# Kernel optimization log

Measured on AMD Instinct MI355X. Metric: run time of the kernel, lower is better.

## Reference

```python
import jax, jax.numpy as jnp
import numpy as np

NPOINT, RADIUS, NSAMPLE = 1024, 0.2, 32
ALPHA, EPS = 0.2, 1e-5  # leaky-relu slope, BN eps


def index_points(points, idx):
    # points [B,N,C], idx [B,...] int -> [B,...,C]
    return jax.vmap(lambda p, i: p[i])(points, idx)


def farthest_point_sample(xyz, npoint):
    # xyz [B,N,3] -> idx [B,npoint]; deterministic start at index 0
    B, N, _ = xyz.shape

    def step(carry, _):
        dist, far = carry
        centroid = jnp.take_along_axis(xyz, far[:, None, None], axis=1)  # [B,1,3]
        d = jnp.sum((xyz - centroid) ** 2, -1)                           # [B,N]
        dist = jnp.minimum(dist, d)
        return (dist, jnp.argmax(dist, -1).astype(jnp.int32)), far

    init = (jnp.full((B, N), 1e10, xyz.dtype), jnp.zeros((B,), jnp.int32))
    _, idxs = jax.lax.scan(step, init, None, length=npoint)
    return idxs.T  # [B, npoint]


def square_distance(src, dst):
    d = -2.0 * jnp.einsum('bnc,bmc->bnm', src, dst)
    d = d + jnp.sum(src ** 2, -1)[:, :, None]
    d = d + jnp.sum(dst ** 2, -1)[:, None, :]
    return d


def query_ball_point(radius, nsample, xyz, new_xyz):
    B, N, _ = xyz.shape
    sqr = square_distance(new_xyz, xyz)  # [B,S,N]
    gi = jnp.where(sqr > radius ** 2, N, jnp.arange(N, dtype=jnp.int32)[None, None, :])
    gi = jnp.sort(gi, axis=-1)[:, :, :nsample]  # [B,S,K]
    first = gi[:, :, :1]
    return jnp.where(gi == N, first, gi)


def mlp_bn_relu(x, W, b, g, be, m, v):
    # 1x1 conv + eval-mode BatchNorm + ReLU; x [..., Cin]
    y = jnp.einsum('...i,oi->...o', x, W) + b
    y = (y - m) * (g / jnp.sqrt(v + EPS)) + be
    return jax.nn.relu(y)


def _forward(xyz, points, W0, b0, g0, be0, m0, v0, W1, b1, g1, be1, m1, v1,
             W2, b2, g2, be2, m2, v2, a):
    xyz_t = jnp.transpose(xyz, (0, 2, 1))     # [B,N,3]
    pts = jnp.transpose(points, (0, 2, 1))    # [B,N,D]

    fps_idx = farthest_point_sample(xyz_t, NPOINT)          # [B,S]
    new_xyz = index_points(xyz_t, fps_idx)                  # [B,S,3]
    idx = query_ball_point(RADIUS, NSAMPLE, xyz_t, new_xyz)  # [B,S,K]
    grouped_xyz = index_points(xyz_t, idx)                  # [B,S,K,3]
    grouped_norm = grouped_xyz - new_xyz[:, :, None, :]
    grouped_pts = index_points(pts, idx)                    # [B,S,K,D]
    fps_points = jnp.concatenate([new_xyz, index_points(pts, fps_idx)], -1)  # [B,S,3+D]
    new_points = jnp.concatenate([grouped_norm, grouped_pts], -1)            # [B,S,K,3+D]

    layers = [(W0, b0, g0, be0, m0, v0), (W1, b1, g1, be1, m1, v1),
              (W2, b2, g2, be2, m2, v2)]
    for (W, b, g, be, m, v) in layers:
        fps_points = mlp_bn_relu(fps_points, W, b, g, be, m, v)
        new_points = mlp_bn_relu(new_points, W, b, g, be, m, v)

    # graph attention pooling over neighbors (dim K)
    delta_p = new_xyz[:, :, None, :] - grouped_xyz                      # [B,S,K,3]
    delta_h = fps_points[:, :, None, :] - new_points                    # [B,S,K,F]
    e = jax.nn.leaky_relu(
        jnp.einsum('bskc,cf->bskf', jnp.concatenate([delta_p, delta_h], -1), a),
        ALPHA)
    att = jax.nn.softmax(e, axis=2)                                     # softmax over K
    pooled = jnp.sum(att * new_points, axis=2)                          # [B,S,F]
    return jnp.transpose(new_xyz, (0, 2, 1)), jnp.transpose(pooled, (0, 2, 1))


def setup_inputs() -> dict:
    key = jax.random.key(0)
    ks = jax.random.split(key, 32)
    d = {}
    d['xyz'] = jax.random.uniform(ks[0], (16, 3, 4096), jnp.float32)
    d['points'] = jax.random.normal(ks[1], (16, 6, 4096), jnp.float32)
    dims = [(9, 64), (64, 64), (64, 128)]
    for li, (ci, co) in enumerate(dims):
        d[f'W{li}'] = jax.random.normal(ks[2 + 6 * li], (co, ci), jnp.float32) * (1.0 / np.sqrt(ci))
        d[f'b{li}'] = jax.random.normal(ks[3 + 6 * li], (co,), jnp.float32) * 0.05
        d[f'g{li}'] = jax.random.uniform(ks[4 + 6 * li], (co,), jnp.float32, 0.5, 1.5)
        d[f'be{li}'] = jax.random.normal(ks[5 + 6 * li], (co,), jnp.float32) * 0.05
        d[f'm{li}'] = jax.random.normal(ks[6 + 6 * li], (co,), jnp.float32) * 0.05
        d[f'v{li}'] = jax.random.uniform(ks[7 + 6 * li], (co,), jnp.float32, 0.5, 1.5)
    d['a'] = jax.random.normal(ks[20], (131, 128), jnp.float32) * 0.1
    return d


def reference(xyz, points, W0, b0, g0, be0, m0, v0, W1, b1, g1, be1, m1, v1,
              W2, b2, g2, be2, m2, v2, a):
    return _forward(xyz, points, W0, b0, g0, be0, m0, v0, W1, b1, g1, be1,
                    m1, v1, W2, b2, g2, be2, m2, v2, a)
```

## Files before the change

### kernel.cpp

```cpp
#include <hip/hip_runtime.h>

#define BB 16
#define NN 4096
#define SS 1024
#define KNB 32

#define FPSIDX_OFF 0
#define GIDX_OFF   (BB*SS)
#define NORM_OFF   (GIDX_OFF + BB*SS*KNB)
#define FPIN_OFF   (NORM_OFF + BB*NN)
#define WF_OFF     (FPIN_OFF + BB*SS*9)

#define W0T 0
#define B0F 576
#define W1T 640
#define B1F 4736
#define W2T 4800
#define B2F 12992

__global__ __launch_bounds__(128) void k_fold(
    const float* W0,const float* b0,const float* g0,const float* be0,const float* m0,const float* v0,
    const float* W1,const float* b1,const float* g1,const float* be1,const float* m1,const float* v1,
    const float* W2,const float* b2,const float* g2,const float* be2,const float* m2,const float* v2,
    float* wf){
  int t = threadIdx.x;
  if (t < 64){
    float s = g0[t]/sqrtf(v0[t]+1e-5f);
    wf[B0F+t] = (b0[t]-m0[t])*s + be0[t];
    for (int c=0;c<9;c++) wf[W0T + c*64 + t] = W0[t*9+c]*s;
    float s1 = g1[t]/sqrtf(v1[t]+1e-5f);
    wf[B1F+t] = (b1[t]-m1[t])*s1 + be1[t];
    for (int c=0;c<64;c++) wf[W1T + c*64 + t] = W1[t*64+c]*s1;
  }
  if (t < 128){
    float s2 = g2[t]/sqrtf(v2[t]+1e-5f);
    wf[B2F+t] = (b2[t]-m2[t])*s2 + be2[t];
    for (int c=0;c<64;c++) wf[W2T + c*128 + t] = W2[t*64+c]*s2;
  }
}

__global__ __launch_bounds__(256) void k_norm(const float* xyz, float* nrm){
  int i = blockIdx.x*256 + threadIdx.x;
  int b = i >> 12, n = i & (NN-1);
  const float* X = xyz + (size_t)b*3*NN;
  float x=X[n], y=X[NN+n], z=X[2*NN+n];
  nrm[i] = __fadd_rn(__fadd_rn(__fmul_rn(x,x),__fmul_rn(y,y)),__fmul_rn(z,z));
}

template<int CTRL, int RMASK>
__device__ __forceinline__ void dpp_max_step(unsigned &lo, unsigned &hi){
  unsigned nlo = (unsigned)__builtin_amdgcn_update_dpp(0, (int)lo, CTRL, RMASK, 0xF, false);
  unsigned nhi = (unsigned)__builtin_amdgcn_update_dpp(0, (int)hi, CTRL, RMASK, 0xF, false);
  unsigned long long cand = ((unsigned long long)nhi<<32) | nlo;
  unsigned long long curk = ((unsigned long long)hi<<32)  | lo;
  if (cand > curk){ lo = nlo; hi = nhi; }
}

__global__ __launch_bounds__(256) void k_fps(const float* xyz, int* fpsidx){
  __shared__ float px[NN], py[NN], pz[NN];
  __shared__ unsigned long long red[2][4];
  int b = blockIdx.x, tid = threadIdx.x;
  int w = tid >> 6, lane = tid & 63;
  const float* X = xyz + (size_t)b*3*NN;
  float lx[16], ly[16], lz[16], dist[16];
  #pragma unroll
  for (int j=0;j<16;j++){
    int p = tid + j*256;
    float x = X[p], y = X[NN+p], z = X[2*NN+p];
    px[p]=x; py[p]=y; pz[p]=z;
    lx[j]=x; ly[j]=y; lz[j]=z; dist[j]=1e10f;
  }
  if (tid==0) fpsidx[b*SS] = 0;
  __syncthreads();
  int cur = 0;
  for (int t=1;t<SS;t++){
    float cx=px[cur], cy=py[cur], cz=pz[cur];
    float bv = -1.0f; int bj = 0;
    #pragma unroll
    for (int j=0;j<16;j++){
      float dx=__fsub_rn(lx[j],cx), dy=__fsub_rn(ly[j],cy), dz=__fsub_rn(lz[j],cz);
      float d = __fadd_rn(__fadd_rn(__fmul_rn(dx,dx),__fmul_rn(dy,dy)),__fmul_rn(dz,dz));
      float nd = fminf(dist[j], d);
      dist[j] = nd;
      bool c = nd > bv;
      bv = c ? nd : bv;
      bj = c ? j  : bj;
    }
    int bi = tid + (bj << 8);
    unsigned lo = 0xFFFFFFFFu - (unsigned)bi;
    unsigned hi = __float_as_uint(bv);
    dpp_max_step<0x111,0xF>(lo,hi);
    dpp_max_step<0x112,0xF>(lo,hi);
    dpp_max_step<0x114,0xF>(lo,hi);
    dpp_max_step<0x118,0xF>(lo,hi);
    dpp_max_step<0x142,0xA>(lo,hi);
    dpp_max_step<0x143,0xC>(lo,hi);
    unsigned glo = (unsigned)__builtin_amdgcn_readlane((int)lo, 63);
    unsigned ghi = (unsigned)__builtin_amdgcn_readlane((int)hi, 63);
    if (lane==0) red[t&1][w] = ((unsigned long long)ghi<<32) | glo;
    __syncthreads();
    unsigned long long k0 = red[t&1][0], k1 = red[t&1][1];
    unsigned long long k2 = red[t&1][2], k3 = red[t&1][3];
    unsigned long long bk = k0;
    if (k1 > bk) bk = k1;
    if (k2 > bk) bk = k2;
    if (k3 > bk) bk = k3;
    cur = (int)(0xFFFFFFFFu - (unsigned)(bk & 0xFFFFFFFFull));
    if (tid==0) fpsidx[b*SS+t] = cur;
  }
}

__global__ __launch_bounds__(256) void k_ball(const float* xyz, const float* points, const float* nrm,
                                              const int* fpsidx, int* gidx, float* fpin, float* out0){
  int wid = threadIdx.x >> 6, lane = threadIdx.x & 63;
  int s = blockIdx.x*4 + wid;
  int b = s >> 10, si = s & (SS-1);
  const float* X = xyz + (size_t)b*3*NN;
  int cidx = fpsidx[s];
  float sx = X[cidx], sy = X[NN+cidx], sz = X[2*NN+cidx];
  float sn = nrm[b*NN + cidx];
  if (lane < 3){
    float v = lane==0?sx:(lane==1?sy:sz);
    fpin[s*9+lane] = v;
    out0[b*3*SS + lane*SS + si] = v;
  } else if (lane < 9){
    fpin[s*9+lane] = points[(size_t)b*6*NN + (size_t)(lane-3)*NN + cidx];
  }
  const float R2 = (float)(0.2*0.2);
  int total = 0; int first = 0;
  for (int ch=0; ch<NN/64; ch++){
    int n = ch*64 + lane;
    float pxv=X[n], pyv=X[NN+n], pzv=X[2*NN+n];
    float dot = __fmaf_rn(sz,pzv, __fmaf_rn(sy,pyv, __fmul_rn(sx,pxv)));
    float sqr = __fadd_rn(__fadd_rn(__fmul_rn(-2.0f,dot), sn), nrm[b*NN+n]);
    bool inc = (sqr <= R2);
    unsigned long long mask = __ballot(inc);
    if (total == 0 && mask != 0ull) first = ch*64 + (__ffsll((long long)mask) - 1);
    if (inc){
      int pos = total + __popcll(mask & ((1ull<<lane)-1ull));
      if (pos < KNB) gidx[s*KNB + pos] = n;
    }
    total += (int)__popcll(mask);
    if (total >= KNB) break;
  }
  if (total < KNB && lane >= total && lane < KNB) gidx[s*KNB + lane] = first;
}

__global__ __launch_bounds__(256) void k_fused(const float* __restrict__ xyz,
                                               const float* __restrict__ points,
                                               const float* __restrict__ am,
                                               const float* __restrict__ wf,
                                               const int* __restrict__ gidx,
                                               const float* __restrict__ fpin,
                                               float* __restrict__ out1){
  __shared__ float smem[64*68*2];
  __shared__ float Hf1[2][64], Hf2[2][64], F3l[2][128];
  float* H1  = smem;
  float* H2  = smem + 64*68;
  float* DNP = smem;

  int tid  = threadIdx.x;
  int lane = tid & 63;
  int k    = lane & 31;
  int ctr  = lane >> 5;
  int wv   = __builtin_amdgcn_readfirstlane(tid >> 6);
  int s0   = blockIdx.x*2;
  int s    = s0 + ctr;
  int b    = s >> 10;
  int si   = s & (SS-1);
  int row  = lane;

  int ki = gidx[s*KNB + k];
  const float* X = xyz + (size_t)b*3*NN;
  const float* P = points + (size_t)b*6*NN;
  float fin0 = fpin[s*9+0], fin1 = fpin[s*9+1], fin2 = fpin[s*9+2];
  float gx0 = X[ki]      - fin0;
  float gx1 = X[NN+ki]   - fin1;
  float gx2 = X[2*NN+ki] - fin2;
  float g3 = P[ki], g4 = P[NN+ki], g5 = P[2*NN+ki];
  float g6 = P[3*NN+ki], g7 = P[4*NN+ki], g8 = P[5*NN+ki];

  {
    int f0 = wv*16;
    float acc[16];
    #pragma unroll
    for (int j=0;j<16;j++) acc[j] = wf[B0F + f0 + j];
    #pragma unroll
    for (int c=0;c<9;c++){
      float xv = (c==0)?gx0:(c==1)?gx1:(c==2)?gx2:(c==3)?g3:(c==4)?g4:(c==5)?g5:(c==6)?g6:(c==7)?g7:g8;
      const float* wr = wf + W0T + c*64 + f0;
      #pragma unroll
      for (int j=0;j<16;j++) acc[j] = fmaf(xv, wr[j], acc[j]);
    }
    #pragma unroll
    for (int j=0;j<16;j+=4){
      float4 o; o.x=fmaxf(acc[j],0.f); o.y=fmaxf(acc[j+1],0.f);
      o.z=fmaxf(acc[j+2],0.f); o.w=fmaxf(acc[j+3],0.f);
      *(float4*)&H1[row*68 + f0 + j] = o;
    }
  }
  if (tid < 128){
    int f = tid & 63; int cf = tid >> 6;
    int sf = s0 + cf;
    float acc = wf[B0F + f];
    #pragma unroll
    for (int c=0;c<9;c++) acc = fmaf(fpin[sf*9+c], wf[W0T + c*64 + f], acc);
    Hf1[cf][f] = fmaxf(acc, 0.0f);
  }
  __syncthreads();

  {
    int f0 = wv*16;
    float acc[16];
    #pragma unroll
    for (int j=0;j<16;j++) acc[j] = wf[B1F + f0 + j];
    #pragma unroll 8
    for (int c4=0;c4<16;c4++){
      float4 hv = *(const float4*)&H1[row*68 + c4*4];
      const float* wr = wf + W1T + c4*4*64 + f0;
      #pragma unroll
      for (int j=0;j<16;j++) acc[j] = fmaf(hv.x, wr[j],     acc[j]);
      #pragma unroll
      for (int j=0;j<16;j++) acc[j] = fmaf(hv.y, wr[64+j],  acc[j]);
      #pragma unroll
      for (int j=0;j<16;j++) acc[j] = fmaf(hv.z, wr[128+j], acc[j]);
      #pragma unroll
      for (int j=0;j<16;j++) acc[j] = fmaf(hv.w, wr[192+j], acc[j]);
    }
    #pragma unroll
    for (int j=0;j<16;j+=4){
      float4 o; o.x=fmaxf(acc[j],0.f); o.y=fmaxf(acc[j+1],0.f);
      o.z=fmaxf(acc[j+2],0.f); o.w=fmaxf(acc[j+3],0.f);
      *(float4*)&H2[row*68 + f0 + j] = o;
    }
  }
  if (tid < 128){
    int f = tid & 63; int cf = tid >> 6;
    float acc = wf[B1F + f];
    #pragma unroll 16
    for (int c=0;c<64;c++) acc = fmaf(Hf1[cf][c], wf[W1T + c*64 + f], acc);
    Hf2[cf][f] = fmaxf(acc, 0.0f);
  }
  __syncthreads();

  float np[32];
  {
    int f0 = wv*32;
    #pragma unroll
    for (int j=0;j<32;j++) np[j] = wf[B2F + f0 + j];
    #pragma unroll 4
    for (int c4=0;c4<16;c4++){
      float4 hv = *(const float4*)&H2[row*68 + c4*4];
      const float* wr = wf + W2T + c4*4*128 + f0;
      #pragma unroll
      for (int j=0;j<32;j++) np[j] = fmaf(hv.x, wr[j],     np[j]);
      #pragma unroll
      for (int j=0;j<32;j++) np[j] = fmaf(hv.y, wr[128+j], np[j]);
      #pragma unroll
      for (int j=0;j<32;j++) np[j] = fmaf(hv.z, wr[256+j], np[j]);
      #pragma unroll
      for (int j=0;j<32;j++) np[j] = fmaf(hv.w, wr[384+j], np[j]);
    }
    #pragma unroll
    for (int j=0;j<32;j++) np[j] = fmaxf(np[j], 0.0f);
  }
  {
    int f = tid & 127; int cf = tid >> 7;
    float acc = wf[B2F + f];
    #pragma unroll 16
    for (int c=0;c<64;c++) acc = fmaf(Hf2[cf][c], wf[W2T + c*128 + f], acc);
    F3l[cf][f] = fmaxf(acc, 0.0f);
  }
  __syncthreads();

  {
    int f0 = wv*32;
    #pragma unroll
    for (int j=0;j<32;j+=4){
      float4 d;
      d.x = F3l[ctr][f0+j]   - np[j];
      d.y = F3l[ctr][f0+j+1] - np[j+1];
      d.z = F3l[ctr][f0+j+2] - np[j+2];
      d.w = F3l[ctr][f0+j+3] - np[j+3];
      *(float4*)&DNP[row*132 + f0 + j] = d;
    }
  }
  __syncthreads();

  {
    float dp0 = -gx0, dp1 = -gx1, dp2 = -gx2;
    size_t ob = (size_t)b*128*SS + si;
    #pragma unroll
    for (int p=0;p<4;p++){
      int f0 = wv*32 + p*8;
      float e[8];
      const float* a0 = am + f0;
      #pragma unroll
      for (int j=0;j<8;j++)
        e[j] = fmaf(dp2, a0[256+j], fmaf(dp1, a0[128+j], dp0*a0[j]));
      #pragma unroll 4
      for (int c4=0;c4<32;c4++){
        float4 dv = *(const float4*)&DNP[row*132 + c4*4];
        const float* wr = am + (3 + c4*4)*128 + f0;
        #pragma unroll
        for (int j=0;j<8;j++) e[j] = fmaf(dv.x, wr[j],     e[j]);
        #pragma unroll
        for (int j=0;j<8;j++) e[j] = fmaf(dv.y, wr[128+j], e[j]);
        #pragma unroll
        for (int j=0;j<8;j++) e[j] = fmaf(dv.z, wr[256+j], e[j]);
        #pragma unroll
        for (int j=0;j<8;j++) e[j] = fmaf(dv.w, wr[384+j], e[j]);
      }
      #pragma unroll
      for (int j=0;j<8;j++){
        float ej = e[j]; ej = (ej >= 0.0f) ? ej : 0.2f*ej;
        float mx = ej;
        mx = fmaxf(mx, __shfl_xor(mx,1));
        mx = fmaxf(mx, __shfl_xor(mx,2));
        mx = fmaxf(mx, __shfl_xor(mx,4));
        mx = fmaxf(mx, __shfl_xor(mx,8));
        mx = fmaxf(mx, __shfl_xor(mx,16));
        float pp = __expf(ej - mx);
        float sm = pp;
        sm += __shfl_xor(sm,1); sm += __shfl_xor(sm,2); sm += __shfl_xor(sm,4);
        sm += __shfl_xor(sm,8); sm += __shfl_xor(sm,16);
        float po = (pp / sm) * np[p*8+j];
        po += __shfl_xor(po,1); po += __shfl_xor(po,2); po += __shfl_xor(po,4);
        po += __shfl_xor(po,8); po += __shfl_xor(po,16);
        if (k == 0) out1[ob + (size_t)(f0+j)*SS] = po;
      }
    }
  }
}

extern "C" void kernel_launch(void* const* d_in, const int* in_sizes, int n_in,
                              void* d_out, int out_size, void* d_ws, size_t ws_size,
                              hipStream_t stream){
  (void)in_sizes; (void)n_in; (void)out_size; (void)ws_size;
  const float* xyz    = (const float*)d_in[0];
  const float* points = (const float*)d_in[1];
  const float* am     = (const float*)d_in[20];
  float* ws  = (float*)d_ws;
  int*   fpsidx = (int*)d_ws + FPSIDX_OFF;
  int*   gidx   = (int*)d_ws + GIDX_OFF;
  float* nrm    = ws + NORM_OFF;
  float* fpin   = ws + FPIN_OFF;
  float* wf     = ws + WF_OFF;
  float* out0   = (float*)d_out;
  float* out1   = (float*)d_out + BB*3*SS;

  k_fold<<<1,128,0,stream>>>(
      (const float*)d_in[2],(const float*)d_in[3],(const float*)d_in[4],(const float*)d_in[5],(const float*)d_in[6],(const float*)d_in[7],
      (const float*)d_in[8],(const float*)d_in[9],(const float*)d_in[10],(const float*)d_in[11],(const float*)d_in[12],(const float*)d_in[13],
      (const float*)d_in[14],(const float*)d_in[15],(const float*)d_in[16],(const float*)d_in[17],(const float*)d_in[18],(const float*)d_in[19],
      wf);
  k_norm<<<BB*NN/256,256,0,stream>>>(xyz, nrm);
  k_fps<<<BB,256,0,stream>>>(xyz, fpsidx);
  k_ball<<<BB*SS/4,256,0,stream>>>(xyz, points, nrm, fpsidx, gidx, fpin, out0);
  k_fused<<<BB*SS/2,256,0,stream>>>(xyz, points, am, wf, gidx, fpin, out1);
}
```

Before: 1.108 ms.

## Widen FPS to 512 threads with packed float2 math and float4 centroid loads

The farthest-point-sampling kernel now runs 512 threads per batch instead of 256, so each thread holds 8 points instead of 16. Distances are computed with two-wide float vectors so the compiler can emit packed FP32 instructions, with contraction disabled to keep rounding exact. The centroid is read as one float4 from shared memory right after the reduction. The aim is a shorter serial per-iteration critical path in this latency-bound 1023-step loop. In exchange the cross-wave reduction is 8-way instead of 4-way, and the barrier now spans 8 waves.

```diff
diff --git a/kernel.cpp b/kernel.cpp
--- a/kernel.cpp
+++ b/kernel.cpp
@@ -17,6 +17,8 @@
 #define B1F 4736
 #define W2T 4800
 #define B2F 12992
+
+typedef float v2f __attribute__((ext_vector_type(2)));
 
 __global__ __launch_bounds__(128) void k_fold(
     const float* W0,const float* b0,const float* g0,const float* be0,const float* m0,const float* v0,
@@ -56,37 +58,46 @@
   if (cand > curk){ lo = nlo; hi = nhi; }
 }
 
-__global__ __launch_bounds__(256) void k_fps(const float* xyz, int* fpsidx){
-  __shared__ float px[NN], py[NN], pz[NN];
-  __shared__ unsigned long long red[2][4];
+__global__ __launch_bounds__(512) void k_fps(const float* xyz, int* fpsidx){
+  #pragma clang fp contract(off)
+  __shared__ float4 pxyz4[NN];
+  __shared__ unsigned long long red[2][8];
   int b = blockIdx.x, tid = threadIdx.x;
   int w = tid >> 6, lane = tid & 63;
   const float* X = xyz + (size_t)b*3*NN;
-  float lx[16], ly[16], lz[16], dist[16];
+  v2f lx[4], ly[4], lz[4], dist[4];
   #pragma unroll
-  for (int j=0;j<16;j++){
-    int p = tid + j*256;
-    float x = X[p], y = X[NN+p], z = X[2*NN+p];
-    px[p]=x; py[p]=y; pz[p]=z;
-    lx[j]=x; ly[j]=y; lz[j]=z; dist[j]=1e10f;
+  for (int m=0;m<4;m++){
+    int p0 = tid + (2*m)*512, p1 = tid + (2*m+1)*512;
+    float x0=X[p0], y0=X[NN+p0], z0=X[2*NN+p0];
+    float x1=X[p1], y1=X[NN+p1], z1=X[2*NN+p1];
+    float4 q0; q0.x=x0; q0.y=y0; q0.z=z0; q0.w=0.f;
+    float4 q1; q1.x=x1; q1.y=y1; q1.z=z1; q1.w=0.f;
+    pxyz4[p0] = q0; pxyz4[p1] = q1;
+    lx[m].x=x0; lx[m].y=x1; ly[m].x=y0; ly[m].y=y1; lz[m].x=z0; lz[m].y=z1;
+    dist[m].x=1e10f; dist[m].y=1e10f;
   }
   if (tid==0) fpsidx[b*SS] = 0;
-  __syncthreads();
-  int cur = 0;
+  float cx = X[0], cy = X[NN], cz = X[2*NN];
+  __syncthreads();
   for (int t=1;t<SS;t++){
-    float cx=px[cur], cy=py[cur], cz=pz[cur];
+    v2f cxx, cyy, czz;
+    cxx.x=cx; cxx.y=cx; cyy.x=cy; cyy.y=cy; czz.x=cz; czz.y=cz;
     float bv = -1.0f; int bj = 0;
     #pragma unroll
-    for (int j=0;j<16;j++){
-      float dx=__fsub_rn(lx[j],cx), dy=__fsub_rn(ly[j],cy), dz=__fsub_rn(lz[j],cz);
-      float d = __fadd_rn(__fadd_rn(__fmul_rn(dx,dx),__fmul_rn(dy,dy)),__fmul_rn(dz,dz));
-      float nd = fminf(dist[j], d);
-      dist[j] = nd;
-      bool c = nd > bv;
-      bv = c ? nd : bv;
-      bj = c ? j  : bj;
-    }
-    int bi = tid + (bj << 8);
+    for (int m=0;m<4;m++){
+      v2f dx = lx[m]-cxx, dy = ly[m]-cyy, dz = lz[m]-czz;
+      v2f dd = (dx*dx + dy*dy) + dz*dz;
+      v2f nd; nd.x = fminf(dist[m].x, dd.x); nd.y = fminf(dist[m].y, dd.y);
+      dist[m] = nd;
+      bool pc = nd.y > nd.x;
+      float vm = pc ? nd.y : nd.x;
+      int   jm = pc ? (2*m+1) : (2*m);
+      bool c = vm > bv;
+      bv = c ? vm : bv;
+      bj = c ? jm : bj;
+    }
+    int bi = tid + (bj << 9);
     unsigned lo = 0xFFFFFFFFu - (unsigned)bi;
     unsigned hi = __float_as_uint(bv);
     dpp_max_step<0x111,0xF>(lo,hi);
@@ -101,11 +112,18 @@
     __syncthreads();
     unsigned long long k0 = red[t&1][0], k1 = red[t&1][1];
     unsigned long long k2 = red[t&1][2], k3 = red[t&1][3];
-    unsigned long long bk = k0;
-    if (k1 > bk) bk = k1;
-    if (k2 > bk) bk = k2;
-    if (k3 > bk) bk = k3;
-    cur = (int)(0xFFFFFFFFu - (unsigned)(bk & 0xFFFFFFFFull));
+    unsigned long long k4 = red[t&1][4], k5 = red[t&1][5];
+    unsigned long long k6 = red[t&1][6], k7 = red[t&1][7];
+    unsigned long long a0 = (k1>k0)?k1:k0;
+    unsigned long long a1 = (k3>k2)?k3:k2;
+    unsigned long long a2 = (k5>k4)?k5:k4;
+    unsigned long long a3 = (k7>k6)?k7:k6;
+    unsigned long long b0 = (a1>a0)?a1:a0;
+    unsigned long long b1 = (a3>a2)?a3:a2;
+    unsigned long long bk = (b1>b0)?b1:b0;
+    int cur = (int)(0xFFFFFFFFu - (unsigned)(bk & 0xFFFFFFFFull));
+    float4 cc = pxyz4[cur];
+    cx = cc.x; cy = cc.y; cz = cc.z;
     if (tid==0) fpsidx[b*SS+t] = cur;
   }
 }
@@ -355,7 +373,7 @@
       (const float*)d_in[14],(const float*)d_in[15],(const float*)d_in[16],(const float*)d_in[17],(const float*)d_in[18],(const float*)d_in[19],
       wf);
   k_norm<<<BB*NN/256,256,0,stream>>>(xyz, nrm);
-  k_fps<<<BB,256,0,stream>>>(xyz, fpsidx);
+  k_fps<<<BB,512,0,stream>>>(xyz, fpsidx);
   k_ball<<<BB*SS/4,256,0,stream>>>(xyz, points, nrm, fpsidx, gidx, fpin, out0);
   k_fused<<<BB*SS/2,256,0,stream>>>(xyz, points, am, wf, gidx, fpin, out1);
 }
```

Measured after the change: 1.200 ms. 8.3% more time.

## Fuse FPS, ball query and MLP into persistent producer-consumer megakernel

Applied to the files above, without the earlier changes.

Merges the FPS, ball-query and fused MLP/attention kernels into a single persistent kernel. Sixteen blocks run FPS and publish each centroid index with atomic stores, while the other 944 blocks spin-wait on those indices so ball query and MLP overlap the serial FPS. The FPS loop now carries the winning point's coordinates through the DPP reduction, which drops the shared-memory coordinate lookup each step. Group indices and centroid features stay in LDS instead of going through global memory. The risks are deadlock if the FPS blocks are not all resident alongside the spinning consumers, and ordering that depends on relaxed atomics.

```diff
diff --git a/kernel.cpp b/kernel.cpp
--- a/kernel.cpp
+++ b/kernel.cpp
@@ -5,11 +5,12 @@
 #define SS 1024
 #define KNB 32
 
+#define NCONS 944
+#define NBLK (NCONS + 16)
+
 #define FPSIDX_OFF 0
-#define GIDX_OFF   (BB*SS)
-#define NORM_OFF   (GIDX_OFF + BB*SS*KNB)
-#define FPIN_OFF   (NORM_OFF + BB*NN)
-#define WF_OFF     (FPIN_OFF + BB*SS*9)
+#define NORM_OFF   (BB*SS)
+#define WF_OFF     (NORM_OFF + BB*NN)
 
 #define W0T 0
 #define B0F 576
@@ -48,288 +49,316 @@
 }
 
 template<int CTRL, int RMASK>
-__device__ __forceinline__ void dpp_max_step(unsigned &lo, unsigned &hi){
-  unsigned nlo = (unsigned)__builtin_amdgcn_update_dpp(0, (int)lo, CTRL, RMASK, 0xF, false);
-  unsigned nhi = (unsigned)__builtin_amdgcn_update_dpp(0, (int)hi, CTRL, RMASK, 0xF, false);
+__device__ __forceinline__ void dpp5(unsigned &klo, unsigned &khi, float &x, float &y, float &z){
+  unsigned nlo = (unsigned)__builtin_amdgcn_update_dpp(0, (int)klo, CTRL, RMASK, 0xF, false);
+  unsigned nhi = (unsigned)__builtin_amdgcn_update_dpp(0, (int)khi, CTRL, RMASK, 0xF, false);
+  int nx = __builtin_amdgcn_update_dpp(0, __float_as_int(x), CTRL, RMASK, 0xF, false);
+  int ny = __builtin_amdgcn_update_dpp(0, __float_as_int(y), CTRL, RMASK, 0xF, false);
+  int nz = __builtin_amdgcn_update_dpp(0, __float_as_int(z), CTRL, RMASK, 0xF, false);
   unsigned long long cand = ((unsigned long long)nhi<<32) | nlo;
-  unsigned long long curk = ((unsigned long long)hi<<32)  | lo;
-  if (cand > curk){ lo = nlo; hi = nhi; }
-}
-
-__global__ __launch_bounds__(256) void k_fps(const float* xyz, int* fpsidx){
-  __shared__ float px[NN], py[NN], pz[NN];
-  __shared__ unsigned long long red[2][4];
-  int b = blockIdx.x, tid = threadIdx.x;
-  int w = tid >> 6, lane = tid & 63;
-  const float* X = xyz + (size_t)b*3*NN;
-  float lx[16], ly[16], lz[16], dist[16];
-  #pragma unroll
-  for (int j=0;j<16;j++){
-    int p = tid + j*256;
-    float x = X[p], y = X[NN+p], z = X[2*NN+p];
-    px[p]=x; py[p]=y; pz[p]=z;
-    lx[j]=x; ly[j]=y; lz[j]=z; dist[j]=1e10f;
-  }
-  if (tid==0) fpsidx[b*SS] = 0;
-  __syncthreads();
-  int cur = 0;
-  for (int t=1;t<SS;t++){
-    float cx=px[cur], cy=py[cur], cz=pz[cur];
-    float bv = -1.0f; int bj = 0;
+  unsigned long long curk = ((unsigned long long)khi<<32) | klo;
+  if (cand > curk){
+    klo=nlo; khi=nhi;
+    x=__int_as_float(nx); y=__int_as_float(ny); z=__int_as_float(nz);
+  }
+}
+
+__global__ __launch_bounds__(256, 4) void k_mega(const float* __restrict__ xyz,
+                                                 const float* __restrict__ points,
+                                                 const float* __restrict__ am,
+                                                 const float* __restrict__ wf,
+                                                 const float* __restrict__ nrm,
+                                                 int* fpsidx,
+                                                 float* __restrict__ out0,
+                                                 float* __restrict__ out1){
+  __shared__ float smem[64*68*2];
+  __shared__ float Hf1[2][64], Hf2[2][64], F3l[2][128];
+  __shared__ int   gidx_l[2][KNB];
+  __shared__ float fpin_l[2][12];
+  __shared__ unsigned long long rkey[2][4];
+  __shared__ float4 rxyz[2][4];
+
+  int tid  = threadIdx.x;
+  int lane = tid & 63;
+  int w    = tid >> 6;
+
+  if (blockIdx.x < 16){
+    int b = blockIdx.x;
+    const float* X = xyz + (size_t)b*3*NN;
+    float lx[16], ly[16], lz[16], dist[16];
     #pragma unroll
     for (int j=0;j<16;j++){
-      float dx=__fsub_rn(lx[j],cx), dy=__fsub_rn(ly[j],cy), dz=__fsub_rn(lz[j],cz);
-      float d = __fadd_rn(__fadd_rn(__fmul_rn(dx,dx),__fmul_rn(dy,dy)),__fmul_rn(dz,dz));
-      float nd = fminf(dist[j], d);
-      dist[j] = nd;
-      bool c = nd > bv;
-      bv = c ? nd : bv;
-      bj = c ? j  : bj;
-    }
-    int bi = tid + (bj << 8);
-    unsigned lo = 0xFFFFFFFFu - (unsigned)bi;
-    unsigned hi = __float_as_uint(bv);
-    dpp_max_step<0x111,0xF>(lo,hi);
-    dpp_max_step<0x112,0xF>(lo,hi);
-    dpp_max_step<0x114,0xF>(lo,hi);
-    dpp_max_step<0x118,0xF>(lo,hi);
-    dpp_max_step<0x142,0xA>(lo,hi);
-    dpp_max_step<0x143,0xC>(lo,hi);
-    unsigned glo = (unsigned)__builtin_amdgcn_readlane((int)lo, 63);
-    unsigned ghi = (unsigned)__builtin_amdgcn_readlane((int)hi, 63);
-    if (lane==0) red[t&1][w] = ((unsigned long long)ghi<<32) | glo;
-    __syncthreads();
-    unsigned long long k0 = red[t&1][0], k1 = red[t&1][1];
-    unsigned long long k2 = red[t&1][2], k3 = red[t&1][3];
-    unsigned long long bk = k0;
-    if (k1 > bk) bk = k1;
-    if (k2 > bk) bk = k2;
-    if (k3 > bk) bk = k3;
-    cur = (int)(0xFFFFFFFFu - (unsigned)(bk & 0xFFFFFFFFull));
-    if (tid==0) fpsidx[b*SS+t] = cur;
-  }
-}
-
-__global__ __launch_bounds__(256) void k_ball(const float* xyz, const float* points, const float* nrm,
-                                              const int* fpsidx, int* gidx, float* fpin, float* out0){
-  int wid = threadIdx.x >> 6, lane = threadIdx.x & 63;
-  int s = blockIdx.x*4 + wid;
-  int b = s >> 10, si = s & (SS-1);
-  const float* X = xyz + (size_t)b*3*NN;
-  int cidx = fpsidx[s];
-  float sx = X[cidx], sy = X[NN+cidx], sz = X[2*NN+cidx];
-  float sn = nrm[b*NN + cidx];
-  if (lane < 3){
-    float v = lane==0?sx:(lane==1?sy:sz);
-    fpin[s*9+lane] = v;
-    out0[b*3*SS + lane*SS + si] = v;
-  } else if (lane < 9){
-    fpin[s*9+lane] = points[(size_t)b*6*NN + (size_t)(lane-3)*NN + cidx];
-  }
-  const float R2 = (float)(0.2*0.2);
-  int total = 0; int first = 0;
-  for (int ch=0; ch<NN/64; ch++){
-    int n = ch*64 + lane;
-    float pxv=X[n], pyv=X[NN+n], pzv=X[2*NN+n];
-    float dot = __fmaf_rn(sz,pzv, __fmaf_rn(sy,pyv, __fmul_rn(sx,pxv)));
-    float sqr = __fadd_rn(__fadd_rn(__fmul_rn(-2.0f,dot), sn), nrm[b*NN+n]);
-    bool inc = (sqr <= R2);
-    unsigned long long mask = __ballot(inc);
-    if (total == 0 && mask != 0ull) first = ch*64 + (__ffsll((long long)mask) - 1);
-    if (inc){
-      int pos = total + __popcll(mask & ((1ull<<lane)-1ull));
-      if (pos < KNB) gidx[s*KNB + pos] = n;
-    }
-    total += (int)__popcll(mask);
-    if (total >= KNB) break;
-  }
-  if (total < KNB && lane >= total && lane < KNB) gidx[s*KNB + lane] = first;
-}
-
-__global__ __launch_bounds__(256) void k_fused(const float* __restrict__ xyz,
-                                               const float* __restrict__ points,
-                                               const float* __restrict__ am,
-                                               const float* __restrict__ wf,
-                                               const int* __restrict__ gidx,
-                                               const float* __restrict__ fpin,
-                                               float* __restrict__ out1){
-  __shared__ float smem[64*68*2];
-  __shared__ float Hf1[2][64], Hf2[2][64], F3l[2][128];
+      int p = tid + j*256;
+      lx[j]=X[p]; ly[j]=X[NN+p]; lz[j]=X[2*NN+p]; dist[j]=1e10f;
+    }
+    if (tid==0)
+      __hip_atomic_store((unsigned*)&fpsidx[b*SS], 0u, __ATOMIC_RELAXED, __HIP_MEMORY_SCOPE_AGENT);
+    float cx = X[0], cy = X[NN], cz = X[2*NN];
+    __syncthreads();
+    for (int t=1;t<SS;t++){
+      float bv = -1.0f, bx = 0.f, by = 0.f, bz = 0.f; int bj = 0;
+      #pragma unroll
+      for (int j=0;j<16;j++){
+        float dx=__fsub_rn(lx[j],cx), dy=__fsub_rn(ly[j],cy), dz=__fsub_rn(lz[j],cz);
+        float d = __fadd_rn(__fadd_rn(__fmul_rn(dx,dx),__fmul_rn(dy,dy)),__fmul_rn(dz,dz));
+        float nd = fminf(dist[j], d);
+        dist[j] = nd;
+        bool c = nd > bv;
+        bv = c ? nd : bv;
+        bj = c ? j  : bj;
+        bx = c ? lx[j] : bx; by = c ? ly[j] : by; bz = c ? lz[j] : bz;
+      }
+      int bi = tid + (bj << 8);
+      unsigned klo = 0xFFFFFFFFu - (unsigned)bi;
+      unsigned khi = __float_as_uint(bv);
+      dpp5<0x111,0xF>(klo,khi,bx,by,bz);
+      dpp5<0x112,0xF>(klo,khi,bx,by,bz);
+      dpp5<0x114,0xF>(klo,khi,bx,by,bz);
+      dpp5<0x118,0xF>(klo,khi,bx,by,bz);
+      dpp5<0x142,0xA>(klo,khi,bx,by,bz);
+      dpp5<0x143,0xC>(klo,khi,bx,by,bz);
+      unsigned glo = (unsigned)__builtin_amdgcn_readlane((int)klo, 63);
+      unsigned ghi = (unsigned)__builtin_amdgcn_readlane((int)khi, 63);
+      float wx = __int_as_float(__builtin_amdgcn_readlane(__float_as_int(bx), 63));
+      float wy = __int_as_float(__builtin_amdgcn_readlane(__float_as_int(by), 63));
+      float wz = __int_as_float(__builtin_amdgcn_readlane(__float_as_int(bz), 63));
+      int par = t & 1;
+      if (lane==0){
+        rkey[par][w] = ((unsigned long long)ghi<<32) | glo;
+        float4 q; q.x=wx; q.y=wy; q.z=wz; q.w=0.f;
+        rxyz[par][w] = q;
+      }
+      __syncthreads();
+      unsigned long long k0 = rkey[par][0], k1 = rkey[par][1];
+      unsigned long long k2 = rkey[par][2], k3 = rkey[par][3];
+      float4 c0 = rxyz[par][0], c1 = rxyz[par][1], c2 = rxyz[par][2], c3 = rxyz[par][3];
+      bool s01 = k1 > k0; unsigned long long a0 = s01?k1:k0;
+      float ax = s01?c1.x:c0.x, ay = s01?c1.y:c0.y, az = s01?c1.z:c0.z;
+      bool s23 = k3 > k2; unsigned long long a1 = s23?k3:k2;
+      float ex = s23?c3.x:c2.x, ey = s23?c3.y:c2.y, ez = s23?c3.z:c2.z;
+      bool sf = a1 > a0; unsigned long long bk = sf?a1:a0;
+      cx = sf?ex:ax; cy = sf?ey:ay; cz = sf?ez:az;
+      int cur = (int)(0xFFFFFFFFu - (unsigned)(bk & 0xFFFFFFFFull));
+      if (tid==0)
+        __hip_atomic_store((unsigned*)&fpsidx[b*SS+t], (unsigned)cur, __ATOMIC_RELAXED, __HIP_MEMORY_SCOPE_AGENT);
+    }
+    return;
+  }
+
+  int j    = blockIdx.x - 16;
+  int k    = lane & 31;
+  int ctr  = lane >> 5;
+  int wv   = __builtin_amdgcn_readfirstlane(tid >> 6);
   float* H1  = smem;
   float* H2  = smem + 64*68;
   float* DNP = smem;
-
-  int tid  = threadIdx.x;
-  int lane = tid & 63;
-  int k    = lane & 31;
-  int ctr  = lane >> 5;
-  int wv   = __builtin_amdgcn_readfirstlane(tid >> 6);
-  int s0   = blockIdx.x*2;
-  int s    = s0 + ctr;
-  int b    = s >> 10;
-  int si   = s & (SS-1);
-  int row  = lane;
-
-  int ki = gidx[s*KNB + k];
-  const float* X = xyz + (size_t)b*3*NN;
-  const float* P = points + (size_t)b*6*NN;
-  float fin0 = fpin[s*9+0], fin1 = fpin[s*9+1], fin2 = fpin[s*9+2];
-  float gx0 = X[ki]      - fin0;
-  float gx1 = X[NN+ki]   - fin1;
-  float gx2 = X[2*NN+ki] - fin2;
-  float g3 = P[ki], g4 = P[NN+ki], g5 = P[2*NN+ki];
-  float g6 = P[3*NN+ki], g7 = P[4*NN+ki], g8 = P[5*NN+ki];
-
-  {
-    int f0 = wv*16;
-    float acc[16];
-    #pragma unroll
-    for (int j=0;j<16;j++) acc[j] = wf[B0F + f0 + j];
-    #pragma unroll
-    for (int c=0;c<9;c++){
-      float xv = (c==0)?gx0:(c==1)?gx1:(c==2)?gx2:(c==3)?g3:(c==4)?g4:(c==5)?g5:(c==6)?g6:(c==7)?g7:g8;
-      const float* wr = wf + W0T + c*64 + f0;
-      #pragma unroll
-      for (int j=0;j<16;j++) acc[j] = fmaf(xv, wr[j], acc[j]);
-    }
-    #pragma unroll
-    for (int j=0;j<16;j+=4){
-      float4 o; o.x=fmaxf(acc[j],0.f); o.y=fmaxf(acc[j+1],0.f);
-      o.z=fmaxf(acc[j+2],0.f); o.w=fmaxf(acc[j+3],0.f);
-      *(float4*)&H1[row*68 + f0 + j] = o;
-    }
-  }
-  if (tid < 128){
-    int f = tid & 63; int cf = tid >> 6;
-    int sf = s0 + cf;
-    float acc = wf[B0F + f];
-    #pragma unroll
-    for (int c=0;c<9;c++) acc = fmaf(fpin[sf*9+c], wf[W0T + c*64 + f], acc);
-    Hf1[cf][f] = fmaxf(acc, 0.0f);
-  }
-  __syncthreads();
-
-  {
-    int f0 = wv*16;
-    float acc[16];
-    #pragma unroll
-    for (int j=0;j<16;j++) acc[j] = wf[B1F + f0 + j];
-    #pragma unroll 8
-    for (int c4=0;c4<16;c4++){
-      float4 hv = *(const float4*)&H1[row*68 + c4*4];
-      const float* wr = wf + W1T + c4*4*64 + f0;
-      #pragma unroll
-      for (int j=0;j<16;j++) acc[j] = fmaf(hv.x, wr[j],     acc[j]);
-      #pragma unroll
-      for (int j=0;j<16;j++) acc[j] = fmaf(hv.y, wr[64+j],  acc[j]);
-      #pragma unroll
-      for (int j=0;j<16;j++) acc[j] = fmaf(hv.z, wr[128+j], acc[j]);
-      #pragma unroll
-      for (int j=0;j<16;j++) acc[j] = fmaf(hv.w, wr[192+j], acc[j]);
-    }
-    #pragma unroll
-    for (int j=0;j<16;j+=4){
-      float4 o; o.x=fmaxf(acc[j],0.f); o.y=fmaxf(acc[j+1],0.f);
-      o.z=fmaxf(acc[j+2],0.f); o.w=fmaxf(acc[j+3],0.f);
-      *(float4*)&H2[row*68 + f0 + j] = o;
-    }
-  }
-  if (tid < 128){
-    int f = tid & 63; int cf = tid >> 6;
-    float acc = wf[B1F + f];
-    #pragma unroll 16
-    for (int c=0;c<64;c++) acc = fmaf(Hf1[cf][c], wf[W1T + c*64 + f], acc);
-    Hf2[cf][f] = fmaxf(acc, 0.0f);
-  }
-  __syncthreads();
-
-  float np[32];
-  {
-    int f0 = wv*32;
-    #pragma unroll
-    for (int j=0;j<32;j++) np[j] = wf[B2F + f0 + j];
-    #pragma unroll 4
-    for (int c4=0;c4<16;c4++){
-      float4 hv = *(const float4*)&H2[row*68 + c4*4];
-      const float* wr = wf + W2T + c4*4*128 + f0;
-      #pragma unroll
-      for (int j=0;j<32;j++) np[j] = fmaf(hv.x, wr[j],     np[j]);
-      #pragma unroll
-      for (int j=0;j<32;j++) np[j] = fmaf(hv.y, wr[128+j], np[j]);
-      #pragma unroll
-      for (int j=0;j<32;j++) np[j] = fmaf(hv.z, wr[256+j], np[j]);
-      #pragma unroll
-      for (int j=0;j<32;j++) np[j] = fmaf(hv.w, wr[384+j], np[j]);
-    }
-    #pragma unroll
-    for (int j=0;j<32;j++) np[j] = fmaxf(np[j], 0.0f);
-  }
-  {
-    int f = tid & 127; int cf = tid >> 7;
-    float acc = wf[B2F + f];
-    #pragma unroll 16
-    for (int c=0;c<64;c++) acc = fmaf(Hf2[cf][c], wf[W2T + c*128 + f], acc);
-    F3l[cf][f] = fmaxf(acc, 0.0f);
-  }
-  __syncthreads();
-
-  {
-    int f0 = wv*32;
-    #pragma unroll
-    for (int j=0;j<32;j+=4){
-      float4 d;
-      d.x = F3l[ctr][f0+j]   - np[j];
-      d.y = F3l[ctr][f0+j+1] - np[j+1];
-      d.z = F3l[ctr][f0+j+2] - np[j+2];
-      d.w = F3l[ctr][f0+j+3] - np[j+3];
-      *(float4*)&DNP[row*132 + f0 + j] = d;
-    }
-  }
-  __syncthreads();
-
-  {
-    float dp0 = -gx0, dp1 = -gx1, dp2 = -gx2;
-    size_t ob = (size_t)b*128*SS + si;
-    #pragma unroll
-    for (int p=0;p<4;p++){
-      int f0 = wv*32 + p*8;
-      float e[8];
-      const float* a0 = am + f0;
-      #pragma unroll
-      for (int j=0;j<8;j++)
-        e[j] = fmaf(dp2, a0[256+j], fmaf(dp1, a0[128+j], dp0*a0[j]));
+  int row = lane;
+
+  for (int u = j; u < BB*SS/2; u += NCONS){
+    int bb = u & 15;
+    int pp = u >> 4;
+    const float* X = xyz + (size_t)bb*3*NN;
+    const float* P = points + (size_t)bb*6*NN;
+
+    if (w < 2){
+      int si = 2*pp + w;
+      int sg = bb*SS + si;
+      int cidx;
+      for(;;){
+        unsigned v = __hip_atomic_load((const unsigned*)&fpsidx[sg], __ATOMIC_RELAXED, __HIP_MEMORY_SCOPE_AGENT);
+        if (v != 0xFFFFFFFFu){ cidx = (int)v; break; }
+        __builtin_amdgcn_s_sleep(4);
+      }
+      float sx = X[cidx], sy = X[NN+cidx], sz = X[2*NN+cidx];
+      float sn = nrm[bb*NN + cidx];
+      if (lane < 3){
+        float v = lane==0?sx:(lane==1?sy:sz);
+        fpin_l[w][lane] = v;
+        out0[bb*3*SS + lane*SS + si] = v;
+      } else if (lane < 9){
+        fpin_l[w][lane] = points[(size_t)bb*6*NN + (size_t)(lane-3)*NN + cidx];
+      }
+      const float R2 = (float)(0.2*0.2);
+      int total = 0; int first = 0;
+      for (int ch=0; ch<NN/64; ch++){
+        int n = ch*64 + lane;
+        float pxv=X[n], pyv=X[NN+n], pzv=X[2*NN+n];
+        float dot = __fmaf_rn(sz,pzv, __fmaf_rn(sy,pyv, __fmul_rn(sx,pxv)));
+        float sqr = __fadd_rn(__fadd_rn(__fmul_rn(-2.0f,dot), sn), nrm[bb*NN+n]);
+        bool inc = (sqr <= R2);
+        unsigned long long mask = __ballot(inc);
+        if (total == 0 && mask != 0ull) first = ch*64 + (__ffsll((long long)mask) - 1);
+        if (inc){
+          int pos = total + __popcll(mask & ((1ull<<lane)-1ull));
+          if (pos < KNB) gidx_l[w][pos] = n;
+        }
+        total += (int)__popcll(mask);
+        if (total >= KNB) break;
+      }
+      if (total < KNB && lane >= total && lane < KNB) gidx_l[w][lane] = first;
+    }
+    __syncthreads();
+
+    int sil = 2*pp + ctr;
+    int ki = gidx_l[ctr][k];
+    float fin0 = fpin_l[ctr][0], fin1 = fpin_l[ctr][1], fin2 = fpin_l[ctr][2];
+    float gx0 = X[ki]      - fin0;
+    float gx1 = X[NN+ki]   - fin1;
+    float gx2 = X[2*NN+ki] - fin2;
+    float g3 = P[ki], g4 = P[NN+ki], g5 = P[2*NN+ki];
+    float g6 = P[3*NN+ki], g7 = P[4*NN+ki], g8 = P[5*NN+ki];
+
+    {
+      int f0 = wv*16;
+      float acc[16];
+      #pragma unroll
+      for (int q=0;q<16;q++) acc[q] = wf[B0F + f0 + q];
+      #pragma unroll
+      for (int c=0;c<9;c++){
+        float xv = (c==0)?gx0:(c==1)?gx1:(c==2)?gx2:(c==3)?g3:(c==4)?g4:(c==5)?g5:(c==6)?g6:(c==7)?g7:g8;
+        const float* wr = wf + W0T + c*64 + f0;
+        #pragma unroll
+        for (int q=0;q<16;q++) acc[q] = fmaf(xv, wr[q], acc[q]);
+      }
+      #pragma unroll
+      for (int q=0;q<16;q+=4){
+        float4 o; o.x=fmaxf(acc[q],0.f); o.y=fmaxf(acc[q+1],0.f);
+        o.z=fmaxf(acc[q+2],0.f); o.w=fmaxf(acc[q+3],0.f);
+        *(float4*)&H1[row*68 + f0 + q] = o;
+      }
+    }
+    if (tid < 128){
+      int f = tid & 63; int cf = tid >> 6;
+      float acc = wf[B0F + f];
+      #pragma unroll
+      for (int c=0;c<9;c++) acc = fmaf(fpin_l[cf][c], wf[W0T + c*64 + f], acc);
+      Hf1[cf][f] = fmaxf(acc, 0.0f);
+    }
+    __syncthreads();
+
+    {
+      int f0 = wv*16;
+      float acc[16];
+      #pragma unroll
+      for (int q=0;q<16;q++) acc[q] = wf[B1F + f0 + q];
+      #pragma unroll 8
+      for (int c4=0;c4<16;c4++){
+        float4 hv = *(const float4*)&H1[row*68 + c4*4];
+        const float* wr = wf + W1T + c4*4*64 + f0;
+        #pragma unroll
+        for (int q=0;q<16;q++) acc[q] = fmaf(hv.x, wr[q],     acc[q]);
+        #pragma unroll
+        for (int q=0;q<16;q++) acc[q] = fmaf(hv.y, wr[64+q],  acc[q]);
+        #pragma unroll
+        for (int q=0;q<16;q++) acc[q] = fmaf(hv.z, wr[128+q], acc[q]);
+        #pragma unroll
+        for (int q=0;q<16;q++) acc[q] = fmaf(hv.w, wr[192+q], acc[q]);
+      }
+      #pragma unroll
+      for (int q=0;q<16;q+=4){
+        float4 o; o.x=fmaxf(acc[q],0.f); o.y=fmaxf(acc[q+1],0.f);
+        o.z=fmaxf(acc[q+2],0.f); o.w=fmaxf(acc[q+3],0.f);
+        *(float4*)&H2[row*68 + f0 + q] = o;
+      }
+    }
+    if (tid < 128){
+      int f = tid & 63; int cf = tid >> 6;
+      float acc = wf[B1F + f];
+      #pragma unroll 16
+      for (int c=0;c<64;c++) acc = fmaf(Hf1[cf][c], wf[W1T + c*64 + f], acc);
+      Hf2[cf][f] = fmaxf(acc, 0.0f);
+    }
+    __syncthreads();
+
+    float np[32];
+    {
+      int f0 = wv*32;
+      #pragma unroll
+      for (int q=0;q<32;q++) np[q] = wf[B2F + f0 + q];
       #pragma unroll 4
-      for (int c4=0;c4<32;c4++){
-        float4 dv = *(const float4*)&DNP[row*132 + c4*4];
-        const float* wr = am + (3 + c4*4)*128 + f0;
-        #pragma unroll
-        for (int j=0;j<8;j++) e[j] = fmaf(dv.x, wr[j],     e[j]);
-        #pragma unroll
-        for (int j=0;j<8;j++) e[j] = fmaf(dv.y, wr[128+j], e[j]);
-        #pragma unroll
-        for (int j=0;j<8;j++) e[j] = fmaf(dv.z, wr[256+j], e[j]);
-        #pragma unroll
-        for (int j=0;j<8;j++) e[j] = fmaf(dv.w, wr[384+j], e[j]);
-      }
-      #pragma unroll
-      for (int j=0;j<8;j++){
-        float ej = e[j]; ej = (ej >= 0.0f) ? ej : 0.2f*ej;
-        float mx = ej;
-        mx = fmaxf(mx, __shfl_xor(mx,1));
-        mx = fmaxf(mx, __shfl_xor(mx,2));
-        mx = fmaxf(mx, __shfl_xor(mx,4));
-        mx = fmaxf(mx, __shfl_xor(mx,8));
-        mx = fmaxf(mx, __shfl_xor(mx,16));
-        float pp = __expf(ej - mx);
-        float sm = pp;
-        sm += __shfl_xor(sm,1); sm += __shfl_xor(sm,2); sm += __shfl_xor(sm,4);
-        sm += __shfl_xor(sm,8); sm += __shfl_xor(sm,16);
-        float po = (pp / sm) * np[p*8+j];
-        po += __shfl_xor(po,1); po += __shfl_xor(po,2); po += __shfl_xor(po,4);
-        po += __shfl_xor(po,8); po += __shfl_xor(po,16);
-        if (k == 0) out1[ob + (size_t)(f0+j)*SS] = po;
-      }
-    }
+      for (int c4=0;c4<16;c4++){
+        float4 hv = *(const float4*)&H2[row*68 + c4*4];
+        const float* wr = wf + W2T + c4*4*128 + f0;
+        #pragma unroll
+        for (int q=0;q<32;q++) np[q] = fmaf(hv.x, wr[q],     np[q]);
+        #pragma unroll
+        for (int q=0;q<32;q++) np[q] = fmaf(hv.y, wr[128+q], np[q]);
+        #pragma unroll
+        for (int q=0;q<32;q++) np[q] = fmaf(hv.z, wr[256+q], np[q]);
+        #pragma unroll
+        for (int q=0;q<32;q++) np[q] = fmaf(hv.w, wr[384+q], np[q]);
+      }
+      #pragma unroll
+      for (int q=0;q<32;q++) np[q] = fmaxf(np[q], 0.0f);
+    }
+    {
+      int f = tid & 127; int cf = tid >> 7;
+      float acc = wf[B2F + f];
+      #pragma unroll 16
+      for (int c=0;c<64;c++) acc = fmaf(Hf2[cf][c], wf[W2T + c*128 + f], acc);
+      F3l[cf][f] = fmaxf(acc, 0.0f);
+    }
+    __syncthreads();
+
+    {
+      int f0 = wv*32;
+      #pragma unroll
+      for (int q=0;q<32;q+=4){
+        float4 d;
+        d.x = F3l[ctr][f0+q]   - np[q];
+        d.y = F3l[ctr][f0+q+1] - np[q+1];
+        d.z = F3l[ctr][f0+q+2] - np[q+2];
+        d.w = F3l[ctr][f0+q+3] - np[q+3];
+        *(float4*)&DNP[row*132 + f0 + q] = d;
+      }
+    }
+    __syncthreads();
+
+    {
+      float dp0 = -gx0, dp1 = -gx1, dp2 = -gx2;
+      size_t ob = (size_t)bb*128*SS + sil;
+      #pragma unroll
+      for (int p=0;p<4;p++){
+        int f0 = wv*32 + p*8;
+        float e[8];
+        const float* a0 = am + f0;
+        #pragma unroll
+        for (int q=0;q<8;q++)
+          e[q] = fmaf(dp2, a0[256+q], fmaf(dp1, a0[128+q], dp0*a0[q]));
+        #pragma unroll 4
+        for (int c4=0;c4<32;c4++){
+          float4 dv = *(const float4*)&DNP[row*132 + c4*4];
+          const float* wr = am + (3 + c4*4)*128 + f0;
+          #pragma unroll
+          for (int q=0;q<8;q++) e[q] = fmaf(dv.x, wr[q],     e[q]);
+          #pragma unroll
+          for (int q=0;q<8;q++) e[q] = fmaf(dv.y, wr[128+q], e[q]);
+          #pragma unroll
+          for (int q=0;q<8;q++) e[q] = fmaf(dv.z, wr[256+q], e[q]);
+          #pragma unroll
+          for (int q=0;q<8;q++) e[q] = fmaf(dv.w, wr[384+q], e[q]);
+        }
+        #pragma unroll
+        for (int q=0;q<8;q++){
+          float ej = e[q]; ej = (ej >= 0.0f) ? ej : 0.2f*ej;
+          float mx = ej;
+          mx = fmaxf(mx, __shfl_xor(mx,1));
+          mx = fmaxf(mx, __shfl_xor(mx,2));
+          mx = fmaxf(mx, __shfl_xor(mx,4));
+          mx = fmaxf(mx, __shfl_xor(mx,8));
+          mx = fmaxf(mx, __shfl_xor(mx,16));
+          float pv = __expf(ej - mx);
+          float sm = pv;
+          sm += __shfl_xor(sm,1); sm += __shfl_xor(sm,2); sm += __shfl_xor(sm,4);
+          sm += __shfl_xor(sm,8); sm += __shfl_xor(sm,16);
+          float po = (pv / sm) * np[p*8+q];
+          po += __shfl_xor(po,1); po += __shfl_xor(po,2); po += __shfl_xor(po,4);
+          po += __shfl_xor(po,8); po += __shfl_xor(po,16);
+          if (k == 0) out1[ob + (size_t)(f0+q)*SS] = po;
+        }
+      }
+    }
+    __syncthreads();
   }
 }
 
@@ -342,12 +371,12 @@
   const float* am     = (const float*)d_in[20];
   float* ws  = (float*)d_ws;
   int*   fpsidx = (int*)d_ws + FPSIDX_OFF;
-  int*   gidx   = (int*)d_ws + GIDX_OFF;
   float* nrm    = ws + NORM_OFF;
-  float* fpin   = ws + FPIN_OFF;
   float* wf     = ws + WF_OFF;
   float* out0   = (float*)d_out;
   float* out1   = (float*)d_out + BB*3*SS;
+
+  hipMemsetAsync(fpsidx, 0xFF, BB*SS*sizeof(int), stream);
 
   k_fold<<<1,128,0,stream>>>(
       (const float*)d_in[2],(const float*)d_in[3],(const float*)d_in[4],(const float*)d_in[5],(const float*)d_in[6],(const float*)d_in[7],
@@ -355,7 +384,5 @@
       (const float*)d_in[14],(const float*)d_in[15],(const float*)d_in[16],(const float*)d_in[17],(const float*)d_in[18],(const float*)d_in[19],
       wf);
   k_norm<<<BB*NN/256,256,0,stream>>>(xyz, nrm);
-  k_fps<<<BB,256,0,stream>>>(xyz, fpsidx);
-  k_ball<<<BB*SS/4,256,0,stream>>>(xyz, points, nrm, fpsidx, gidx, fpin, out0);
-  k_fused<<<BB*SS/2,256,0,stream>>>(xyz, points, am, wf, gidx, fpin, out1);
-}
+  k_mega<<<NBLK,256,0,stream>>>(xyz, points, am, wf, nrm, fpsidx, out0, out1);
+}
```

Measured after the change: 1.180 ms. +6.5%, slower.
